# Performance work log

Hardware: AMD Instinct MI355X
Metric: run time of the kernel (lower is better)

The kernel has to match this reference:

```python
import jax, jax.numpy as jnp
import numpy as np

B, N, D, H = 8, 1024, 768, 12
HD = D // H


def setup_inputs() -> dict:
    key = jax.random.key(0)
    ks = jax.random.split(key, 9)
    s = 1.0 / np.sqrt(D)
    return {
        "x": jax.random.normal(ks[0], (B, N, D), dtype=jnp.float32),
        "Wq": jax.random.normal(ks[1], (D, D), dtype=jnp.float32) * s,
        "bq": jax.random.normal(ks[2], (D,), dtype=jnp.float32) * 0.01,
        "Wk": jax.random.normal(ks[3], (D, D), dtype=jnp.float32) * s,
        "bk": jax.random.normal(ks[4], (D,), dtype=jnp.float32) * 0.01,
        "Wv": jax.random.normal(ks[5], (D, D), dtype=jnp.float32) * s,
        "bv": jax.random.normal(ks[6], (D,), dtype=jnp.float32) * 0.01,
        "Wo": jax.random.normal(ks[7], (D, D), dtype=jnp.float32) * s,
        "bo": jax.random.normal(ks[8], (D,), dtype=jnp.float32) * 0.01,
    }


def reference(x, Wq, bq, Wk, bk, Wv, bv, Wo, bo):
    b, n, d = x.shape
    split = lambda t: t.reshape(b, n, H, HD).transpose(0, 2, 1, 3)  # b h n d
    q = split(x @ Wq + bq)
    k = split(x @ Wk + bk)
    v = split(x @ Wv + bv)
    energy = jnp.einsum('bhqd,bhkd->bhqk', q, k)
    # NOTE: module scales AFTER softmax by sqrt(emb_size) (not head_dim) -- faithful.
    att = jax.nn.softmax(energy, axis=-1) / jnp.sqrt(jnp.float32(D)).astype(x.dtype)
    out = jnp.einsum('bhqk,bhkd->bhqd', att, v)
    out = out.transpose(0, 2, 1, 3).reshape(b, n, d)
    return out @ Wo + bo
```

## Files before the change

### kernel.cpp

```cpp
#include <hip/hip_runtime.h>

#define B_  8
#define N_  1024
#define D_  768
#define H_  12
#define HD_ 64
#define M_  (B_ * N_)
#define WELEM (D_ * D_)
#define XELEM ((size_t)M_ * D_)

typedef _Float16 f16;
typedef f16   f16x8  __attribute__((ext_vector_type(8)));
typedef short bf16x8 __attribute__((ext_vector_type(8)));
typedef float f32x4  __attribute__((ext_vector_type(4)));
typedef unsigned short u16;

__device__ __forceinline__ u16 f2bf(float f) {
    unsigned int x = __float_as_uint(f);
    return (u16)((x + 0x7fffu + ((x >> 16) & 1u)) >> 16);
}
__device__ __forceinline__ u16 f2h(float f) {
    return __builtin_bit_cast(u16, (f16)f);
}
__device__ __forceinline__ unsigned int cvtpk_bf16(float lo, float hi) {
    unsigned int r;
    asm("v_cvt_pk_bf16_f32 %0, %1, %2" : "=v"(r) : "v"(lo), "v"(hi));
    return r;
}
#if __has_builtin(__builtin_amdgcn_exp2f)
#define EXP2F(x) __builtin_amdgcn_exp2f(x)
#else
#define EXP2F(x) exp2f(x)
#endif

#define LOG2E_   1.4426950408889634f
#define EXPBIAS_ 28.853900817779268f

typedef __attribute__((address_space(3))) unsigned int       as3_u32;
typedef __attribute__((address_space(1))) const unsigned int as1_u32;
__device__ __forceinline__ void dma16(const void* g, void* l) {
    __builtin_amdgcn_global_load_lds((as1_u32*)g, (as3_u32*)l, 16, 0, 0);
}

__global__ __launch_bounds__(256) void cvt_x(const float* __restrict__ X,
                                             u16* __restrict__ Xh) {
    int idx = blockIdx.x * 256 + threadIdx.x;
    float4 v = ((const float4*)X)[idx];
    ushort4 o = {f2h(v.x), f2h(v.y), f2h(v.z), f2h(v.w)};
    ((ushort4*)Xh)[idx] = o;
}

__global__ __launch_bounds__(256) void cvt_w(
    const float* __restrict__ w0, const float* __restrict__ w1,
    const float* __restrict__ w2, const float* __restrict__ w3,
    u16* __restrict__ Wt) {
    const float* W = blockIdx.y == 0 ? w0 : blockIdx.y == 1 ? w1
                   : blockIdx.y == 2 ? w2 : w3;
    u16* dst = Wt + (size_t)blockIdx.y * WELEM;
    const int t  = threadIdx.x;
    const int tk = (blockIdx.x % 12) * 64, tn = (blockIdx.x / 12) * 64;
    __shared__ __align__(16) float tile[64][68];
#pragma unroll
    for (int i = 0; i < 4; ++i) {
        int r = (t >> 4) + i * 16, c4 = (t & 15) * 4;
        float4 v = *(const float4*)(W + (size_t)(tk + r) * D_ + tn + c4);
        *(float4*)&tile[r][c4] = v;
    }
    __syncthreads();
#pragma unroll
    for (int i = 0; i < 4; ++i) {
        int nr = (t >> 4) + i * 16, kc = (t & 15) * 4;
        ushort4 o = {f2h(tile[kc + 0][nr]), f2h(tile[kc + 1][nr]),
                     f2h(tile[kc + 2][nr]), f2h(tile[kc + 3][nr])};
        *(ushort4*)(dst + (size_t)(tn + nr) * D_ + tk + kc) = o;
    }
}

__global__ __launch_bounds__(256) void gemm_qkv(
    const u16* __restrict__ Xh, const u16* __restrict__ Wt,
    const float* __restrict__ bq, const float* __restrict__ bk,
    const float* __restrict__ bv, u16* __restrict__ Qf,
    u16* __restrict__ Kf, u16* __restrict__ Vt) {
    __shared__ __align__(16) u16 As[2][128 * 64];
    __shared__ __align__(16) u16 Bs[2][64 * 64];

    const int id  = blockIdx.x;
    const int xcd = id & 7, idx = id >> 3;
    const int m0  = (xcd * 8 + idx / 36) * 128;
    const int rem = idx % 36;
    const int z   = rem / 12, n0 = (rem % 12) * 64;

    const u16* Wz = Wt + (size_t)z * WELEM;
    const float* bias = z == 0 ? bq : z == 1 ? bk : bv;

    const int t = threadIdx.x, lane = t & 63, w = t >> 6;
    const int wm = w >> 1, wn = w & 1;
    const int quad = lane >> 4, ln = lane & 15;
    const int drow = lane >> 3, dcl = (lane & 7) ^ ((lane >> 3) & 7);

#pragma unroll
    for (int j = 0; j < 4; ++j) {
        int i = w * 4 + j, row = i * 8 + drow;
        dma16(Xh + (size_t)(m0 + row) * D_ + dcl * 8, &As[0][i * 512]);
    }
#pragma unroll
    for (int j = 0; j < 2; ++j) {
        int i = w * 2 + j, row = i * 8 + drow;
        dma16(Wz + (size_t)(n0 + row) * D_ + dcl * 8, &Bs[0][i * 512]);
    }

    f32x4 acc[4][2] = {};
#pragma unroll 2
    for (int kk = 0; kk < 12; ++kk) {
        const int cur = kk & 1;
        asm volatile("s_waitcnt vmcnt(0)" ::: "memory");
        __builtin_amdgcn_s_barrier();
        __builtin_amdgcn_sched_barrier(0);
        if (kk < 11) {
            const int k1 = (kk + 1) * 64;
#pragma unroll
            for (int j = 0; j < 4; ++j) {
                int i = w * 4 + j, row = i * 8 + drow;
                dma16(Xh + (size_t)(m0 + row) * D_ + k1 + dcl * 8,
                      &As[cur ^ 1][i * 512]);
            }
#pragma unroll
            for (int j = 0; j < 2; ++j) {
                int i = w * 2 + j, row = i * 8 + drow;
                dma16(Wz + (size_t)(n0 + row) * D_ + k1 + dcl * 8,
                      &Bs[cur ^ 1][i * 512]);
            }
        }
        f16x8 a[4][2], b[2][2];
#pragma unroll
        for (int mt = 0; mt < 4; ++mt)
#pragma unroll
            for (int ks = 0; ks < 2; ++ks)
                a[mt][ks] = *(const f16x8*)&As[cur][(wm * 64 + mt * 16 + ln) * 64 +
                                                    (((ks * 4 + quad) ^ (ln & 7)) * 8)];
#pragma unroll
        for (int nt = 0; nt < 2; ++nt)
#pragma unroll
            for (int ks = 0; ks < 2; ++ks)
                b[nt][ks] = *(const f16x8*)&Bs[cur][(wn * 32 + nt * 16 + ln) * 64 +
                                                    (((ks * 4 + quad) ^ (ln & 7)) * 8)];
#pragma unroll
        for (int mt = 0; mt < 4; ++mt)
#pragma unroll
            for (int nt = 0; nt < 2; ++nt) {
                acc[mt][nt] = __builtin_amdgcn_mfma_f32_16x16x32_f16(
                    a[mt][0], b[nt][0], acc[mt][nt], 0, 0, 0);
                acc[mt][nt] = __builtin_amdgcn_mfma_f32_16x16x32_f16(
                    a[mt][1], b[nt][1], acc[mt][nt], 0, 0, 0);
            }
    }
    const int h = n0 >> 6;
#pragma unroll
    for (int nt = 0; nt < 2; ++nt) {
        int hd = wn * 32 + nt * 16 + ln;
        float bv_ = bias[n0 + hd];
#pragma unroll
        for (int mt = 0; mt < 4; ++mt) {
            int mb = m0 + wm * 64 + mt * 16 + quad * 4;
            int bb = mb >> 10, ns = mb & 1023;
            if (z == 0) {
#pragma unroll
                for (int r = 0; r < 4; ++r)
                    Qf[(((size_t)bb * H_ + h) * N_ + ns + r) * HD_ + hd] =
                        f2h((acc[mt][nt][r] + bv_) * LOG2E_);
            } else if (z == 1) {
#pragma unroll
                for (int r = 0; r < 4; ++r)
                    Kf[(((size_t)bb * H_ + h) * N_ + ns + r) * HD_ + hd] =
                        f2h(acc[mt][nt][r] + bv_);
            } else {
                ushort4 o = {f2bf(acc[mt][nt][0] + bv_), f2bf(acc[mt][nt][1] + bv_),
                             f2bf(acc[mt][nt][2] + bv_), f2bf(acc[mt][nt][3] + bv_)};
                *(ushort4*)(Vt + (((size_t)bb * H_ + h) * HD_ + hd) * N_ + ns) = o;
            }
        }
    }
}

__global__ __launch_bounds__(256) void attn_mfma(
    const u16* __restrict__ Qg, const u16* __restrict__ Kg,
    const u16* __restrict__ Vtg, u16* __restrict__ Og) {
    __shared__ __align__(16) u16 Ks[2][64 * 64];
    __shared__ __align__(16) u16 Vs[2][64 * 64];
    __shared__ __align__(16) u16 Ps[128 * 72];

    const int t = threadIdx.x, lane = t & 63, w = t >> 6;
    const int quad = lane >> 4, ln = lane & 15;
    const int drow = lane >> 3, dcl = (lane & 7) ^ ((lane >> 3) & 7);
    const int id  = blockIdx.x;
    const int id2 = (id & 7) * 96 + (id >> 3);
    const int bh  = id2 >> 3, qt = id2 & 7;
    const u16* Qh  = Qg  + ((size_t)bh * N_ + qt * 128) * HD_;
    const u16* Kh  = Kg  + (size_t)bh * N_ * HD_;
    const u16* Vth = Vtg + (size_t)bh * HD_ * N_;
    u16*       Oh  = Og  + ((size_t)bh * N_ + qt * 128) * HD_;

    const int rho0 = (w * 2 + 0) * 8 + drow;
    const int rho1 = (w * 2 + 1) * 8 + drow;
    const int gk0  = 4 * (rho0 & 15) + (rho0 >> 4);
    const int gk1  = 4 * (rho1 & 15) + (rho1 >> 4);

    f16x8 aq[2][2];
#pragma unroll
    for (int mt = 0; mt < 2; ++mt)
#pragma unroll
        for (int ks = 0; ks < 2; ++ks)
            aq[mt][ks] = *(const f16x8*)(Qh + (size_t)(w * 32 + mt * 16 + ln) * HD_ +
                                         ks * 32 + quad * 8);

    const bf16x8 pone = {0x3F80, 0x3F80, 0x3F80, 0x3F80,
                         0x3F80, 0x3F80, 0x3F80, 0x3F80};
    const f32x4 nb = {-EXPBIAS_, -EXPBIAS_, -EXPBIAS_, -EXPBIAS_};

    f32x4 oacc[2][4] = {};
    f32x4 lacc[2] = {};

    dma16(Kh + (size_t)gk0 * HD_ + dcl * 8, &Ks[0][(w * 2 + 0) * 512]);
    dma16(Kh + (size_t)gk1 * HD_ + dcl * 8, &Ks[0][(w * 2 + 1) * 512]);
    dma16(Vth + (size_t)rho0 * N_ + dcl * 8, &Vs[0][(w * 2 + 0) * 512]);
    dma16(Vth + (size_t)rho1 * N_ + dcl * 8, &Vs[0][(w * 2 + 1) * 512]);

#pragma unroll 2
    for (int kt = 0; kt < 16; ++kt) {
        const int cur = kt & 1;
        asm volatile("s_waitcnt vmcnt(0)" ::: "memory");
        __builtin_amdgcn_s_barrier();
        __builtin_amdgcn_sched_barrier(0);
        if (kt < 15) {
            const int nk = (kt + 1) * 64;
            dma16(Kh + (size_t)(nk + gk0) * HD_ + dcl * 8, &Ks[cur ^ 1][(w * 2 + 0) * 512]);
            dma16(Kh + (size_t)(nk + gk1) * HD_ + dcl * 8, &Ks[cur ^ 1][(w * 2 + 1) * 512]);
            dma16(Vth + (size_t)rho0 * N_ + nk + dcl * 8, &Vs[cur ^ 1][(w * 2 + 0) * 512]);
            dma16(Vth + (size_t)rho1 * N_ + nk + dcl * 8, &Vs[cur ^ 1][(w * 2 + 1) * 512]);
        }

        f32x4 sf[2][4];
        __builtin_amdgcn_s_setprio(1);
#pragma unroll
        for (int nt = 0; nt < 4; ++nt) {
            f16x8 b0 = *(const f16x8*)&Ks[cur][(nt * 16 + ln) * 64 + ((quad) ^ (ln & 7)) * 8];
            f16x8 b1 = *(const f16x8*)&Ks[cur][(nt * 16 + ln) * 64 + ((4 + quad) ^ (ln & 7)) * 8];
#pragma unroll
            for (int mt = 0; mt < 2; ++mt) {
                sf[mt][nt] = __builtin_amdgcn_mfma_f32_16x16x32_f16(aq[mt][0], b0, nb, 0, 0, 0);
                sf[mt][nt] = __builtin_amdgcn_mfma_f32_16x16x32_f16(aq[mt][1], b1, sf[mt][nt], 0, 0, 0);
            }
        }
        __builtin_amdgcn_s_setprio(0);

#pragma unroll
        for (int mt = 0; mt < 2; ++mt)
#pragma unroll
            for (int r = 0; r < 4; ++r) {
                float e0 = EXP2F(sf[mt][0][r]);
                float e1 = EXP2F(sf[mt][1][r]);
                float e2 = EXP2F(sf[mt][2][r]);
                float e3 = EXP2F(sf[mt][3][r]);
                uint2 pk;
                pk.x = cvtpk_bf16(e0, e1);
                pk.y = cvtpk_bf16(e2, e3);
                int q = w * 32 + mt * 16 + quad * 4 + r;
                *(uint2*)&Ps[q * 72 + ln * 4] = pk;
            }

        __builtin_amdgcn_s_setprio(1);
#pragma unroll
        for (int mt = 0; mt < 2; ++mt) {
            bf16x8 ap0 = *(const bf16x8*)&Ps[(w * 32 + mt * 16 + ln) * 72 + quad * 8];
            bf16x8 ap1 = *(const bf16x8*)&Ps[(w * 32 + mt * 16 + ln) * 72 + 32 + quad * 8];
            lacc[mt] = __builtin_amdgcn_mfma_f32_16x16x32_bf16(ap0, pone, lacc[mt], 0, 0, 0);
            lacc[mt] = __builtin_amdgcn_mfma_f32_16x16x32_bf16(ap1, pone, lacc[mt], 0, 0, 0);
#pragma unroll
            for (int nt = 0; nt < 4; ++nt) {
                bf16x8 bv0 = *(const bf16x8*)&Vs[cur][(nt * 16 + ln) * 64 +
                                                      ((quad ^ (ln & 7)) * 8)];
                oacc[mt][nt] = __builtin_amdgcn_mfma_f32_16x16x32_bf16(
                    ap0, bv0, oacc[mt][nt], 0, 0, 0);
                bf16x8 bv1 = *(const bf16x8*)&Vs[cur][(nt * 16 + ln) * 64 +
                                                      (((4 + quad) ^ (ln & 7)) * 8)];
                oacc[mt][nt] = __builtin_amdgcn_mfma_f32_16x16x32_bf16(
                    ap1, bv1, oacc[mt][nt], 0, 0, 0);
            }
        }
        __builtin_amdgcn_s_setprio(0);
    }

    const float sc = 0.036084391824351615f;
#pragma unroll
    for (int mt = 0; mt < 2; ++mt)
#pragma unroll
        for (int r = 0; r < 4; ++r) {
            float inv = sc / lacc[mt][r];
#pragma unroll
            for (int nt = 0; nt < 4; ++nt)
                Oh[(size_t)(w * 32 + mt * 16 + quad * 4 + r) * HD_ + nt * 16 + ln] =
                    f2h(oacc[mt][nt][r] * inv);
        }
}

__global__ __launch_bounds__(256) void gemm_out(
    const u16* __restrict__ Ob, const u16* __restrict__ Wto,
    const float* __restrict__ bias, float* __restrict__ Out) {
    __shared__ __align__(16) u16 As[2][128 * 64];
    __shared__ __align__(16) u16 Bs[2][64 * 64];

    const int id  = blockIdx.x;
    const int id2 = (id & 7) * 96 + (id >> 3);
    const int m0  = (id2 / 12) * 128, n0 = (id2 % 12) * 64;

    const int t = threadIdx.x, lane = t & 63, w = t >> 6;
    const int wm = w >> 1, wn = w & 1;
    const int quad = lane >> 4, ln = lane & 15;
    const int drow = lane >> 3, dcl = (lane & 7) ^ ((lane >> 3) & 7);

#pragma unroll
    for (int j = 0; j < 4; ++j) {
        int i = w * 4 + j, row = i * 8 + drow;
        int m = m0 + row, bb = m >> 10, ns = m & 1023;
        dma16(Ob + (((size_t)bb * H_ + 0) * N_ + ns) * HD_ + dcl * 8, &As[0][i * 512]);
    }
#pragma unroll
    for (int j = 0; j < 2; ++j) {
        int i = w * 2 + j, row = i * 8 + drow;
        dma16(Wto + (size_t)(n0 + row) * D_ + dcl * 8, &Bs[0][i * 512]);
    }

    f32x4 acc[4][2] = {};
#pragma unroll 2
    for (int kk = 0; kk < 12; ++kk) {
        const int cur = kk & 1;
        asm volatile("s_waitcnt vmcnt(0)" ::: "memory");
        __builtin_amdgcn_s_barrier();
        __builtin_amdgcn_sched_barrier(0);
        if (kk < 11) {
            const int head = kk + 1, k1 = head * 64;
#pragma unroll
            for (int j = 0; j < 4; ++j) {
                int i = w * 4 + j, row = i * 8 + drow;
                int m = m0 + row, bb = m >> 10, ns = m & 1023;
                dma16(Ob + (((size_t)bb * H_ + head) * N_ + ns) * HD_ + dcl * 8,
                      &As[cur ^ 1][i * 512]);
            }
#pragma unroll
            for (int j = 0; j < 2; ++j) {
                int i = w * 2 + j, row = i * 8 + drow;
                dma16(Wto + (size_t)(n0 + row) * D_ + k1 + dcl * 8,
                      &Bs[cur ^ 1][i * 512]);
            }
        }
        f16x8 a[4][2], b[2][2];
#pragma unroll
        for (int mt = 0; mt < 4; ++mt)
#pragma unroll
            for (int ks = 0; ks < 2; ++ks)
                a[mt][ks] = *(const f16x8*)&As[cur][(wm * 64 + mt * 16 + ln) * 64 +
                                                    (((ks * 4 + quad) ^ (ln & 7)) * 8)];
#pragma unroll
        for (int nt = 0; nt < 2; ++nt)
#pragma unroll
            for (int ks = 0; ks < 2; ++ks)
                b[nt][ks] = *(const f16x8*)&Bs[cur][(wn * 32 + nt * 16 + ln) * 64 +
                                                    (((ks * 4 + quad) ^ (ln & 7)) * 8)];
#pragma unroll
        for (int mt = 0; mt < 4; ++mt)
#pragma unroll
            for (int nt = 0; nt < 2; ++nt) {
                acc[mt][nt] = __builtin_amdgcn_mfma_f32_16x16x32_f16(
                    a[mt][0], b[nt][0], acc[mt][nt], 0, 0, 0);
                acc[mt][nt] = __builtin_amdgcn_mfma_f32_16x16x32_f16(
                    a[mt][1], b[nt][1], acc[mt][nt], 0, 0, 0);
            }
    }
#pragma unroll
    for (int nt = 0; nt < 2; ++nt) {
        int n = n0 + wn * 32 + nt * 16 + ln;
        float bv_ = bias[n];
#pragma unroll
        for (int mt = 0; mt < 4; ++mt) {
            int mb = m0 + wm * 64 + mt * 16 + quad * 4;
#pragma unroll
            for (int r = 0; r < 4; ++r)
                Out[(size_t)(mb + r) * D_ + n] = acc[mt][nt][r] + bv_;
        }
    }
}

extern "C" void kernel_launch(void* const* d_in, const int* in_sizes, int n_in,
                              void* d_out, int out_size, void* d_ws, size_t ws_size,
                              hipStream_t stream) {
    const float* x  = (const float*)d_in[0];
    const float* Wq = (const float*)d_in[1];
    const float* bq = (const float*)d_in[2];
    const float* Wk = (const float*)d_in[3];
    const float* bk = (const float*)d_in[4];
    const float* Wv = (const float*)d_in[5];
    const float* bv = (const float*)d_in[6];
    const float* Wo = (const float*)d_in[7];
    const float* bo = (const float*)d_in[8];

    u16* Xh = (u16*)d_ws;
    u16* Wt = Xh + XELEM;
    u16* Qf = Wt + 4 * (size_t)WELEM;
    u16* Kf = Qf + XELEM;
    u16* Vt = Kf + XELEM;
    u16* Ob = Vt + XELEM;

    cvt_x<<<dim3((int)(XELEM / 4 / 256)), 256, 0, stream>>>(x, Xh);
    cvt_w<<<dim3(144, 4), 256, 0, stream>>>(Wq, Wk, Wv, Wo, Wt);
    gemm_qkv<<<dim3(2304), 256, 0, stream>>>(Xh, Wt, bq, bk, bv, Qf, Kf, Vt);
    attn_mfma<<<dim3(768), 256, 0, stream>>>(Qf, Kf, Vt, Ob);
    gemm_out<<<dim3(768), 256, 0, stream>>>(
        Ob, Wt + 3 * (size_t)WELEM, bo, (float*)d_out);
}
```

Baseline: 199.4 us.

## Issue next-tile DMA before waiting and replace row-sum MFMA with VALU sums

In all three kernels the next tile's global-to-LDS loads are now issued before the wait, and the wait uses a partial vmcnt so only the current tile must have landed. A second barrier at the end of each iteration keeps the buffer being overwritten safe. In attention, the softmax row-sum MFMAs against a ones vector are replaced by scalar accumulation of the bf16-rounded probabilities plus a cross-lane shuffle reduction at the end. The exp bias moves from the MFMA accumulator init into the exp argument. This adds one barrier per iteration and some VALU work, in exchange for better overlap of loads with MFMA work and fewer MFMA instructions.

```diff
diff --git a/kernel.cpp b/kernel.cpp
--- a/kernel.cpp
+++ b/kernel.cpp
@@ -113,9 +113,6 @@
 #pragma unroll 2
     for (int kk = 0; kk < 12; ++kk) {
         const int cur = kk & 1;
-        asm volatile("s_waitcnt vmcnt(0)" ::: "memory");
-        __builtin_amdgcn_s_barrier();
-        __builtin_amdgcn_sched_barrier(0);
         if (kk < 11) {
             const int k1 = (kk + 1) * 64;
 #pragma unroll
@@ -130,7 +127,13 @@
                 dma16(Wz + (size_t)(n0 + row) * D_ + k1 + dcl * 8,
                       &Bs[cur ^ 1][i * 512]);
             }
-        }
+            asm volatile("s_waitcnt vmcnt(6)" ::: "memory");
+        } else {
+            asm volatile("s_waitcnt vmcnt(0)" ::: "memory");
+        }
+        __builtin_amdgcn_s_barrier();
+        __builtin_amdgcn_sched_barrier(0);
+
         f16x8 a[4][2], b[2][2];
 #pragma unroll
         for (int mt = 0; mt < 4; ++mt)
@@ -153,6 +156,8 @@
                 acc[mt][nt] = __builtin_amdgcn_mfma_f32_16x16x32_f16(
                     a[mt][1], b[nt][1], acc[mt][nt], 0, 0, 0);
             }
+        __builtin_amdgcn_sched_barrier(0);
+        __builtin_amdgcn_s_barrier();
     }
     const int h = n0 >> 6;
 #pragma unroll
@@ -213,12 +218,8 @@
             aq[mt][ks] = *(const f16x8*)(Qh + (size_t)(w * 32 + mt * 16 + ln) * HD_ +
                                          ks * 32 + quad * 8);
 
-    const bf16x8 pone = {0x3F80, 0x3F80, 0x3F80, 0x3F80,
-                         0x3F80, 0x3F80, 0x3F80, 0x3F80};
-    const f32x4 nb = {-EXPBIAS_, -EXPBIAS_, -EXPBIAS_, -EXPBIAS_};
-
+    float lsum[2][4] = {};
     f32x4 oacc[2][4] = {};
-    f32x4 lacc[2] = {};
 
     dma16(Kh + (size_t)gk0 * HD_ + dcl * 8, &Ks[0][(w * 2 + 0) * 512]);
     dma16(Kh + (size_t)gk1 * HD_ + dcl * 8, &Ks[0][(w * 2 + 1) * 512]);
@@ -228,16 +229,18 @@
 #pragma unroll 2
     for (int kt = 0; kt < 16; ++kt) {
         const int cur = kt & 1;
-        asm volatile("s_waitcnt vmcnt(0)" ::: "memory");
-        __builtin_amdgcn_s_barrier();
-        __builtin_amdgcn_sched_barrier(0);
         if (kt < 15) {
             const int nk = (kt + 1) * 64;
             dma16(Kh + (size_t)(nk + gk0) * HD_ + dcl * 8, &Ks[cur ^ 1][(w * 2 + 0) * 512]);
             dma16(Kh + (size_t)(nk + gk1) * HD_ + dcl * 8, &Ks[cur ^ 1][(w * 2 + 1) * 512]);
             dma16(Vth + (size_t)rho0 * N_ + nk + dcl * 8, &Vs[cur ^ 1][(w * 2 + 0) * 512]);
             dma16(Vth + (size_t)rho1 * N_ + nk + dcl * 8, &Vs[cur ^ 1][(w * 2 + 1) * 512]);
-        }
+            asm volatile("s_waitcnt vmcnt(4)" ::: "memory");
+        } else {
+            asm volatile("s_waitcnt vmcnt(0)" ::: "memory");
+        }
+        __builtin_amdgcn_s_barrier();
+        __builtin_amdgcn_sched_barrier(0);
 
         f32x4 sf[2][4];
         __builtin_amdgcn_s_setprio(1);
@@ -247,7 +250,8 @@
             f16x8 b1 = *(const f16x8*)&Ks[cur][(nt * 16 + ln) * 64 + ((4 + quad) ^ (ln & 7)) * 8];
 #pragma unroll
             for (int mt = 0; mt < 2; ++mt) {
-                sf[mt][nt] = __builtin_amdgcn_mfma_f32_16x16x32_f16(aq[mt][0], b0, nb, 0, 0, 0);
+                f32x4 zz = {};
+                sf[mt][nt] = __builtin_amdgcn_mfma_f32_16x16x32_f16(aq[mt][0], b0, zz, 0, 0, 0);
                 sf[mt][nt] = __builtin_amdgcn_mfma_f32_16x16x32_f16(aq[mt][1], b1, sf[mt][nt], 0, 0, 0);
             }
         }
@@ -257,15 +261,19 @@
         for (int mt = 0; mt < 2; ++mt)
 #pragma unroll
             for (int r = 0; r < 4; ++r) {
-                float e0 = EXP2F(sf[mt][0][r]);
-                float e1 = EXP2F(sf[mt][1][r]);
-                float e2 = EXP2F(sf[mt][2][r]);
-                float e3 = EXP2F(sf[mt][3][r]);
+                float e0 = EXP2F(sf[mt][0][r] - EXPBIAS_);
+                float e1 = EXP2F(sf[mt][1][r] - EXPBIAS_);
+                float e2 = EXP2F(sf[mt][2][r] - EXPBIAS_);
+                float e3 = EXP2F(sf[mt][3][r] - EXPBIAS_);
                 uint2 pk;
                 pk.x = cvtpk_bf16(e0, e1);
                 pk.y = cvtpk_bf16(e2, e3);
                 int q = w * 32 + mt * 16 + quad * 4 + r;
                 *(uint2*)&Ps[q * 72 + ln * 4] = pk;
+                lsum[mt][r] += __uint_as_float(pk.x << 16) +
+                               __uint_as_float(pk.x & 0xffff0000u) +
+                               __uint_as_float(pk.y << 16) +
+                               __uint_as_float(pk.y & 0xffff0000u);
             }
 
         __builtin_amdgcn_s_setprio(1);
@@ -273,8 +281,6 @@
         for (int mt = 0; mt < 2; ++mt) {
             bf16x8 ap0 = *(const bf16x8*)&Ps[(w * 32 + mt * 16 + ln) * 72 + quad * 8];
             bf16x8 ap1 = *(const bf16x8*)&Ps[(w * 32 + mt * 16 + ln) * 72 + 32 + quad * 8];
-            lacc[mt] = __builtin_amdgcn_mfma_f32_16x16x32_bf16(ap0, pone, lacc[mt], 0, 0, 0);
-            lacc[mt] = __builtin_amdgcn_mfma_f32_16x16x32_bf16(ap1, pone, lacc[mt], 0, 0, 0);
 #pragma unroll
             for (int nt = 0; nt < 4; ++nt) {
                 bf16x8 bv0 = *(const bf16x8*)&Vs[cur][(nt * 16 + ln) * 64 +
@@ -288,6 +294,8 @@
             }
         }
         __builtin_amdgcn_s_setprio(0);
+        __builtin_amdgcn_sched_barrier(0);
+        __builtin_amdgcn_s_barrier();
     }
 
     const float sc = 0.036084391824351615f;
@@ -295,7 +303,12 @@
     for (int mt = 0; mt < 2; ++mt)
 #pragma unroll
         for (int r = 0; r < 4; ++r) {
-            float inv = sc / lacc[mt][r];
+            float l = lsum[mt][r];
+            l += __shfl_xor(l, 1);
+            l += __shfl_xor(l, 2);
+            l += __shfl_xor(l, 4);
+            l += __shfl_xor(l, 8);
+            float inv = sc / l;
 #pragma unroll
             for (int nt = 0; nt < 4; ++nt)
                 Oh[(size_t)(w * 32 + mt * 16 + quad * 4 + r) * HD_ + nt * 16 + ln] =
@@ -334,9 +347,6 @@
 #pragma unroll 2
     for (int kk = 0; kk < 12; ++kk) {
         const int cur = kk & 1;
-        asm volatile("s_waitcnt vmcnt(0)" ::: "memory");
-        __builtin_amdgcn_s_barrier();
-        __builtin_amdgcn_sched_barrier(0);
         if (kk < 11) {
             const int head = kk + 1, k1 = head * 64;
 #pragma unroll
@@ -352,7 +362,13 @@
                 dma16(Wto + (size_t)(n0 + row) * D_ + k1 + dcl * 8,
                       &Bs[cur ^ 1][i * 512]);
             }
-        }
+            asm volatile("s_waitcnt vmcnt(6)" ::: "memory");
+        } else {
+            asm volatile("s_waitcnt vmcnt(0)" ::: "memory");
+        }
+        __builtin_amdgcn_s_barrier();
+        __builtin_amdgcn_sched_barrier(0);
+
         f16x8 a[4][2], b[2][2];
 #pragma unroll
         for (int mt = 0; mt < 4; ++mt)
@@ -375,6 +391,8 @@
                 acc[mt][nt] = __builtin_amdgcn_mfma_f32_16x16x32_f16(
                     a[mt][1], b[nt][1], acc[mt][nt], 0, 0, 0);
             }
+        __builtin_amdgcn_sched_barrier(0);
+        __builtin_amdgcn_s_barrier();
     }
 #pragma unroll
     for (int nt = 0; nt < 2; ++nt) {
```

Measured after the change: 213.0 us. 6.9% more time.
